# Performance work log

Measured on AMD Instinct MI355X. Metric: run time of the kernel, lower is better.

Reference implementation:

```python
import jax, jax.numpy as jnp
import numpy as np

N = 20000   # nodes
E = 200000  # edges / 1-cells
D = 128     # feature dim
NNZ = 400000
L = 3       # conv layers


def setup_inputs() -> dict:
    key = jax.random.key(0)
    ks = jax.random.split(key, 16)
    s = 1.0 / np.sqrt(D)
    return {
        "x": jax.random.normal(ks[0], (N, D), jnp.float32),
        "xe": jax.random.normal(ks[1], (E, D), jnp.float32),
        "gnn_W": jax.random.normal(ks[2], (L, D, D), jnp.float32) * s,
        "cwnn_W0": jax.random.normal(ks[3], (L, D, D), jnp.float32) * s,
        "cwnn_W1": jax.random.normal(ks[4], (L, D, D), jnp.float32) * s,
        "cwnn_W2": jax.random.normal(ks[5], (L, D, D), jnp.float32) * s,
        "Ldo_val": jax.random.normal(ks[6], (NNZ,), jnp.float32) * 0.1,
        "Lup_val": jax.random.normal(ks[7], (NNZ,), jnp.float32) * 0.1,
        "edges": jax.random.randint(ks[8], (2, E), 0, N, jnp.int32),
        "row": jax.random.randint(ks[9], (E,), 0, N, jnp.int32),
        "col": jax.random.randint(ks[10], (E,), 0, N, jnp.int32),
        "Ldo_idx": jax.random.randint(ks[11], (2, NNZ), 0, E, jnp.int32),
        "Lup_idx": jax.random.randint(ks[12], (2, NNZ), 0, E, jnp.int32),
    }


def _spmm(idx, val, h, n_rows):
    # sparse (COO) matrix @ dense: out[r] = sum_k val[k] * h[idx_col[k]] for idx_row[k]==r
    msgs = val[:, None] * h[idx[1]]             # [nnz, D]
    return jax.ops.segment_sum(msgs, idx[0], num_segments=n_rows)


def reference(x, xe, gnn_W, cwnn_W0, cwnn_W1, cwnn_W2, Ldo_val, Lup_val,
              edges, row, col, Ldo_idx, Lup_idx):
    n = x.shape[0]
    src, dst = edges[0], edges[1]

    # --- GNN over nodes: h' = (h + scatter_sum(h[src] -> dst)) @ W ---
    h = x
    for i in range(gnn_W.shape[0]):
        agg = jax.ops.segment_sum(h[src], dst, num_segments=n)
        h = (h + agg) @ gnn_W[i]
        if i < gnn_W.shape[0] - 1:
            h = jax.nn.relu(h)
    h = jax.nn.relu(h)  # .relu() in CellNetwork.forward

    # --- CWNN over cells: he' = he@W0 + Ldo@(he@W1) + Lup@(he@W2) ---
    he = xe
    for i in range(cwnn_W0.shape[0]):
        he = (he @ cwnn_W0[i]
              + _spmm(Ldo_idx, Ldo_val, he @ cwnn_W1[i], he.shape[0])
              + _spmm(Lup_idx, Lup_val, he @ cwnn_W2[i], he.shape[0]))
        if i < cwnn_W0.shape[0] - 1:
            he = jax.nn.relu(he)
    he = jax.nn.relu(he)  # .relu() in CellNetwork.forward

    # --- dual scatter-add of cell features to nodes + concat ---
    xed = (jax.ops.segment_sum(he, row, num_segments=n)
           + jax.ops.segment_sum(he, col, num_segments=n))
    return jnp.concatenate([h, xed], axis=-1)  # [N, 2D]
```

## Files before the change

kernel.cpp:

```cpp
#include <hip/hip_runtime.h>
#include <cstddef>
#include <cstdint>


using bf16x8 = __attribute__((ext_vector_type(8))) short;
using f32x4  = __attribute__((ext_vector_type(4))) float;
typedef unsigned short u16;
typedef unsigned int   u32;

static inline int cdiv_h(int a, int b){ return (a + b - 1) / b; }

__device__ inline float bflo(u32 u){ return __uint_as_float(u << 16); }
__device__ inline float bfhi(u32 u){ return __uint_as_float(u & 0xFFFF0000u); }
__device__ inline u32 f2bf(float f){
  u32 u = __float_as_uint(f);
  return (u + 0x7FFFu + ((u >> 16) & 1u)) >> 16;
}
__device__ inline u32 pack2(float a, float b){ return f2bf(a) | (f2bf(b) << 16); }


__global__ void hist_key(const int* __restrict__ keys, int* __restrict__ counts, int n){
  int i = blockIdx.x * blockDim.x + threadIdx.x;
  if (i < n) atomicAdd(&counts[keys[i]], 1);
}

__global__ void hist_two(const int* __restrict__ a, const int* __restrict__ b,
                         int* __restrict__ counts, int n){
  int i = blockIdx.x * blockDim.x + threadIdx.x;
  if (i < n){ atomicAdd(&counts[a[i]], 1); atomicAdd(&counts[b[i]], 1); }
}

#define SCAN_CHUNK 2048

__global__ void scan_local(const int* __restrict__ cnt, int* __restrict__ offs,
                           int* __restrict__ partials, int n){
  __shared__ int sd[256];
  int t = threadIdx.x;
  int base = blockIdx.x * SCAN_CHUNK + t * 8;
  int v[8]; int sum = 0;
  #pragma unroll
  for (int i = 0; i < 8; i++){ int idx = base + i; v[i] = (idx < n) ? cnt[idx] : 0; sum += v[i]; }
  sd[t] = sum; __syncthreads();
  for (int off = 1; off < 256; off <<= 1){
    int x = (t >= off) ? sd[t - off] : 0;
    __syncthreads();
    sd[t] += x;
    __syncthreads();
  }
  if (t == 255) partials[blockIdx.x] = sd[255];
  int run = sd[t] - sum;
  #pragma unroll
  for (int i = 0; i < 8; i++){ int idx = base + i; if (idx < n) offs[idx] = run; run += v[i]; }
}

__global__ void scan_partials_k(int* partials, int nb){
  __shared__ int sd[256];
  int t = threadIdx.x;
  int orig = (t < nb) ? partials[t] : 0;
  sd[t] = orig; __syncthreads();
  for (int off = 1; off < 256; off <<= 1){
    int x = (t >= off) ? sd[t - off] : 0;
    __syncthreads();
    sd[t] += x;
    __syncthreads();
  }
  if (t < nb) partials[t] = sd[t] - orig;
}

__global__ void scan_add(int* __restrict__ offs, const int* __restrict__ partials,
                         int n, int total){
  int i = blockIdx.x * blockDim.x + threadIdx.x;
  if (i < n) offs[i] += partials[i / SCAN_CHUNK];
  if (i == 0) offs[n] = total;
}

__global__ void fill_plain(const int* __restrict__ keys, const int* __restrict__ vals,
                           int* __restrict__ cursor, int* __restrict__ ent, int n){
  int i = blockIdx.x * blockDim.x + threadIdx.x;
  if (i < n){ int p = atomicAdd(&cursor[keys[i]], 1); ent[p] = vals[i]; }
}

__global__ void fill_wval(const int* __restrict__ rows, const int* __restrict__ cols,
                          const float* __restrict__ v, int* __restrict__ cursor,
                          int* __restrict__ entc, float* __restrict__ entv, int n){
  int i = blockIdx.x * blockDim.x + threadIdx.x;
  if (i < n){
    int p = atomicAdd(&cursor[rows[i]], 1);
    entc[p] = cols[i]; entv[p] = v[i];
  }
}

__global__ void fill_two(const int* __restrict__ a, const int* __restrict__ b,
                         int* __restrict__ cursor, int* __restrict__ ent, int n){
  int i = blockIdx.x * blockDim.x + threadIdx.x;
  if (i < n){
    int p = atomicAdd(&cursor[a[i]], 1); ent[p] = i;
    int q = atomicAdd(&cursor[b[i]], 1); ent[q] = i;
  }
}


__global__ void gather_f32(const float* __restrict__ src, float* __restrict__ out,
                           const int* __restrict__ offs, const int* __restrict__ ent,
                           const float* __restrict__ selfsrc, int nrows){
  int r = blockIdx.x * 8 + (threadIdx.x >> 5);
  if (r >= nrows) return;
  int d4 = (threadIdx.x & 31) * 4;
  float4 acc0, acc1 = make_float4(0.f, 0.f, 0.f, 0.f);
  acc0 = *(const float4*)&selfsrc[(size_t)r * 128 + d4];
  int b = offs[r], e = offs[r + 1];
  int j = b;
  for (; j + 1 < e; j += 2){
    int c0 = ent[j], c1 = ent[j + 1];
    float4 s0 = *(const float4*)&src[(size_t)c0 * 128 + d4];
    float4 s1 = *(const float4*)&src[(size_t)c1 * 128 + d4];
    acc0.x += s0.x; acc0.y += s0.y; acc0.z += s0.z; acc0.w += s0.w;
    acc1.x += s1.x; acc1.y += s1.y; acc1.z += s1.z; acc1.w += s1.w;
  }
  if (j < e){
    int c = ent[j];
    float4 s = *(const float4*)&src[(size_t)c * 128 + d4];
    acc0.x += s.x; acc0.y += s.y; acc0.z += s.z; acc0.w += s.w;
  }
  acc0.x += acc1.x; acc0.y += acc1.y; acc0.z += acc1.z; acc0.w += acc1.w;
  *(float4*)&out[(size_t)r * 128 + d4] = acc0;
}


__global__ void gather_bf16(const u16* __restrict__ src, u16* __restrict__ out,
                            const int* __restrict__ offs, const int* __restrict__ ent,
                            const float* __restrict__ evals, int nrows){
  int r = blockIdx.x * 8 + (threadIdx.x >> 5);
  if (r >= nrows) return;
  int d4 = (threadIdx.x & 31) * 4;
  float a0=0.f,a1=0.f,a2=0.f,a3=0.f, b0=0.f,b1=0.f,b2=0.f,b3=0.f;
  int b = offs[r], e = offs[r + 1];
  int j = b;
  for (; j + 1 < e; j += 2){
    int c0 = ent[j], c1 = ent[j + 1];
    float w0 = evals[j], w1 = evals[j + 1];
    uint2 s0 = *(const uint2*)&src[(size_t)c0 * 128 + d4];
    uint2 s1 = *(const uint2*)&src[(size_t)c1 * 128 + d4];
    a0 += w0 * bflo(s0.x); a1 += w0 * bfhi(s0.x); a2 += w0 * bflo(s0.y); a3 += w0 * bfhi(s0.y);
    b0 += w1 * bflo(s1.x); b1 += w1 * bfhi(s1.x); b2 += w1 * bflo(s1.y); b3 += w1 * bfhi(s1.y);
  }
  if (j < e){
    int c = ent[j];
    float w = evals[j];
    uint2 s = *(const uint2*)&src[(size_t)c * 128 + d4];
    a0 += w * bflo(s.x); a1 += w * bfhi(s.x); a2 += w * bflo(s.y); a3 += w * bfhi(s.y);
  }
  a0 += b0; a1 += b1; a2 += b2; a3 += b3;
  uint2 o; o.x = pack2(a0, a1); o.y = pack2(a2, a3);
  *(uint2*)&out[(size_t)r * 128 + d4] = o;
}

__global__ void gather_final(const u16* __restrict__ src, float* __restrict__ out,
                             const int* __restrict__ offs, const int* __restrict__ ent,
                             int nrows, int ldout){
  int r = blockIdx.x * 8 + (threadIdx.x >> 5);
  if (r >= nrows) return;
  int d4 = (threadIdx.x & 31) * 4;
  float a0=0.f,a1=0.f,a2=0.f,a3=0.f, b0=0.f,b1=0.f,b2=0.f,b3=0.f;
  int b = offs[r], e = offs[r + 1];
  int j = b;
  for (; j + 1 < e; j += 2){
    int c0 = ent[j], c1 = ent[j + 1];
    uint2 s0 = *(const uint2*)&src[(size_t)c0 * 128 + d4];
    uint2 s1 = *(const uint2*)&src[(size_t)c1 * 128 + d4];
    a0 += bflo(s0.x); a1 += bfhi(s0.x); a2 += bflo(s0.y); a3 += bfhi(s0.y);
    b0 += bflo(s1.x); b1 += bfhi(s1.x); b2 += bflo(s1.y); b3 += bfhi(s1.y);
  }
  if (j < e){
    int c = ent[j];
    uint2 s = *(const uint2*)&src[(size_t)c * 128 + d4];
    a0 += bflo(s.x); a1 += bfhi(s.x); a2 += bflo(s.y); a3 += bfhi(s.y);
  }
  float4 o = make_float4(a0 + b0, a1 + b1, a2 + b2, a3 + b3);
  *(float4*)&out[(size_t)r * ldout + d4] = o;
}


__global__ void cvt_f32_bf16(const float* __restrict__ src, u16* __restrict__ dst, int n8){
  int i = blockIdx.x * blockDim.x + threadIdx.x;
  if (i >= n8) return;
  const float4* s = (const float4*)(src + (size_t)i * 8);
  float4 a = s[0], c = s[1];
  *(uint4*)(dst + (size_t)i * 8) =
      make_uint4(pack2(a.x, a.y), pack2(a.z, a.w), pack2(c.x, c.y), pack2(c.z, c.w));
}


__global__ __launch_bounds__(256) void gemm_f32(
    const float* __restrict__ in, const float* __restrict__ W,
    float* __restrict__ out, int M, int ldout){
  __shared__ float sA[32][132];
  __shared__ float sW[32][128];
  int t  = threadIdx.x;
  int m0 = blockIdx.x * 128;
  int rg = t >> 4;
  int cg = t & 15;
  float acc[8][8];
  #pragma unroll
  for (int i = 0; i < 8; i++)
    #pragma unroll
    for (int j = 0; j < 8; j++) acc[i][j] = 0.f;

  for (int kc = 0; kc < 128; kc += 32){
    #pragma unroll
    for (int ii = 0; ii < 4; ii++){
      int s  = t + ii * 256;
      int r  = s >> 3;
      int k4 = (s & 7) << 2;
      int gr = m0 + r;
      float4 v = (gr < M) ? *(const float4*)&in[(size_t)gr * 128 + kc + k4]
                          : make_float4(0.f, 0.f, 0.f, 0.f);
      sA[k4 + 0][r] = v.x; sA[k4 + 1][r] = v.y; sA[k4 + 2][r] = v.z; sA[k4 + 3][r] = v.w;
    }
    #pragma unroll
    for (int ii = 0; ii < 4; ii++){
      int s  = t + ii * 256;
      int kr = s >> 5;
      int c4 = (s & 31) << 2;
      *(float4*)&sW[kr][c4] = *(const float4*)&W[(size_t)(kc + kr) * 128 + c4];
    }
    __syncthreads();
    #pragma unroll
    for (int k = 0; k < 32; k++){
      float4 a0 = *(const float4*)&sA[k][rg * 8];
      float4 a1 = *(const float4*)&sA[k][rg * 8 + 4];
      float4 w0 = *(const float4*)&sW[k][cg * 8];
      float4 w1 = *(const float4*)&sW[k][cg * 8 + 4];
      float a[8] = {a0.x, a0.y, a0.z, a0.w, a1.x, a1.y, a1.z, a1.w};
      float w[8] = {w0.x, w0.y, w0.z, w0.w, w1.x, w1.y, w1.z, w1.w};
      #pragma unroll
      for (int i = 0; i < 8; i++)
        #pragma unroll
        for (int j = 0; j < 8; j++)
          acc[i][j] = fmaf(a[i], w[j], acc[i][j]);
    }
    __syncthreads();
  }
  #pragma unroll
  for (int i = 0; i < 8; i++){
    int gr = m0 + rg * 8 + i;
    if (gr >= M) continue;
    float* op = out + (size_t)gr * ldout + cg * 8;
    #pragma unroll
    for (int jj = 0; jj < 8; jj += 4){
      float4 o = make_float4(fmaxf(acc[i][jj], 0.f), fmaxf(acc[i][jj + 1], 0.f),
                             fmaxf(acc[i][jj + 2], 0.f), fmaxf(acc[i][jj + 3], 0.f));
      *(float4*)&op[jj] = o;
    }
  }
}


template<int NS>
__global__ __launch_bounds__(256) void gemm_mfma(
    const u16* __restrict__ A0, const u16* __restrict__ A1, const u16* __restrict__ A2,
    const u16* __restrict__ Wa, const u16* __restrict__ Wb, const u16* __restrict__ Wc,
    u16* __restrict__ out, int M){
  __shared__ __align__(16) u16 sA[128 * 40];
  __shared__ __align__(16) u16 sW[128 * 40];
  const int t    = threadIdx.x;
  const int m0   = blockIdx.x * 128;
  const int wid  = t >> 6;
  const int lane = t & 63;
  const int l16  = lane & 15;
  const int kg   = lane >> 4;
  const int nW   = t & 127;
  const int kq   = t >> 7;

  f32x4 acc[2][8];
  #pragma unroll
  for (int i = 0; i < 2; i++)
    #pragma unroll
    for (int j = 0; j < 8; j++) acc[i][j] = (f32x4){0.f, 0.f, 0.f, 0.f};

  #pragma unroll 1
  for (int s = 0; s < NS; s++){
    const u16* A = (s == 0) ? A0 : (s == 1) ? A1 : A2;
    const u16* W = (s == 0) ? Wa : (s == 1) ? Wb : Wc;
    #pragma unroll 1
    for (int kc = 0; kc < 128; kc += 32){
      #pragma unroll
      for (int ii = 0; ii < 2; ii++){
        int sl = t + ii * 256;
        int r  = sl >> 2;
        int q  = sl & 3;
        int gr = m0 + r;
        uint4 v = make_uint4(0u, 0u, 0u, 0u);
        if (gr < M) v = *(const uint4*)&A[(size_t)gr * 128 + kc + q * 8];
        *(uint4*)&sA[r * 40 + q * 8] = v;
      }
      {
        __align__(16) u16 wt[16];
        #pragma unroll
        for (int kk = 0; kk < 16; kk++)
          wt[kk] = W[(size_t)(kc + kq * 16 + kk) * 128 + nW];
        *(uint4*)&sW[nW * 40 + kq * 16]     = *(uint4*)&wt[0];
        *(uint4*)&sW[nW * 40 + kq * 16 + 8] = *(uint4*)&wt[8];
      }
      __syncthreads();
      bf16x8 af0 = *(const bf16x8*)&sA[(wid * 32 +      l16) * 40 + kg * 8];
      bf16x8 af1 = *(const bf16x8*)&sA[(wid * 32 + 16 + l16) * 40 + kg * 8];
      #pragma unroll
      for (int ct = 0; ct < 8; ct++){
        bf16x8 bq = *(const bf16x8*)&sW[(ct * 16 + l16) * 40 + kg * 8];
        acc[0][ct] = __builtin_amdgcn_mfma_f32_16x16x32_bf16(af0, bq, acc[0][ct], 0, 0, 0);
        acc[1][ct] = __builtin_amdgcn_mfma_f32_16x16x32_bf16(af1, bq, acc[1][ct], 0, 0, 0);
      }
      __syncthreads();
    }
  }
  #pragma unroll
  for (int rt = 0; rt < 2; rt++){
    #pragma unroll
    for (int reg = 0; reg < 4; reg++){
      int row = m0 + wid * 32 + rt * 16 + kg * 4 + reg;
      if (row < M){
        #pragma unroll
        for (int ct = 0; ct < 8; ct++){
          float v = fmaxf(acc[rt][ct][reg], 0.f);
          out[(size_t)row * 128 + ct * 16 + l16] = (u16)f2bf(v);
        }
      }
    }
  }
}


extern "C" void kernel_launch(void* const* d_in, const int* in_sizes, int n_in,
                              void* d_out, int out_size, void* d_ws, size_t ws_size,
                              hipStream_t stream){
  const float* x    = (const float*)d_in[0];
  const float* xe   = (const float*)d_in[1];
  const float* gW   = (const float*)d_in[2];
  const float* W0   = (const float*)d_in[3];
  const float* W1   = (const float*)d_in[4];
  const float* W2   = (const float*)d_in[5];
  const float* ldoV = (const float*)d_in[6];
  const float* lupV = (const float*)d_in[7];
  const int*   edges= (const int*)d_in[8];
  const int*   rowi = (const int*)d_in[9];
  const int*   coli = (const int*)d_in[10];
  const int*   ldoI = (const int*)d_in[11];
  const int*   lupI = (const int*)d_in[12];
  (void)n_in; (void)out_size;

  const int D   = 128;
  const int N   = in_sizes[0] / D;
  const int E   = in_sizes[1] / D;
  const int NNZ = in_sizes[6];
  const int L   = in_sizes[2] / (D * D);

  const int* srcN = edges;
  const int* dstN = edges + E;
  const int* ldoR = ldoI;   const int* ldoC = ldoI + NNZ;
  const int* lupR = lupI;   const int* lupC = lupI + NNZ;

  size_t off = 0;
  auto carve = [&](size_t bytes) -> void* {
    void* p = (char*)d_ws + off;
    off += (bytes + 255) & ~(size_t)255;
    return p;
  };
  const size_t EBH = (size_t)E * D * 2;
  u16* EA  = (u16*)carve(EBH);
  u16* EC  = (u16*)carve(EBH);
  u16* EG1 = (u16*)carve(EBH);
  u16* EG2 = (u16*)carve(EBH);
  float* hA = (float*)carve((size_t)N * D * 4);
  float* hB = (float*)carve((size_t)N * D * 4);
  int* offs_g = (int*)carve((size_t)(N + 1) * 4);
  int* cnt_g  = (int*)carve((size_t)N * 4);
  int* ent_g  = (int*)carve((size_t)E * 4);
  int* offs_d = (int*)carve((size_t)(E + 1) * 4);
  int* cnt_d  = (int*)carve((size_t)E * 4);
  int* entc_d = (int*)carve((size_t)NNZ * 4);
  float* entv_d = (float*)carve((size_t)NNZ * 4);
  int* offs_u = (int*)carve((size_t)(E + 1) * 4);
  int* cnt_u  = (int*)carve((size_t)E * 4);
  int* entc_u = (int*)carve((size_t)NNZ * 4);
  float* entv_u = (float*)carve((size_t)NNZ * 4);
  int* offs_f = (int*)carve((size_t)(N + 1) * 4);
  int* cnt_f  = (int*)carve((size_t)N * 4);
  int* ent_f  = (int*)carve((size_t)2 * E * 4);
  int* partials = (int*)carve(256 * 4);
  if (off > ws_size) return;

  const size_t DD = (size_t)D * D;
  u16* WB0 = (u16*)hA;
  u16* WB1 = WB0 + (size_t)L * DD;
  u16* WB2 = WB1 + (size_t)L * DD;

  auto scan3 = [&](int* cnt, int* offs, int n, int total){
    int nb = (n + SCAN_CHUNK - 1) / SCAN_CHUNK;
    scan_local<<<nb, 256, 0, stream>>>(cnt, offs, partials, n);
    scan_partials_k<<<1, 256, 0, stream>>>(partials, nb);
    scan_add<<<cdiv_h(n, 256), 256, 0, stream>>>(offs, partials, n, total);
  };

  hipMemsetAsync(cnt_g, 0, (size_t)N * 4, stream);
  hist_key<<<cdiv_h(E, 256), 256, 0, stream>>>(dstN, cnt_g, E);
  scan3(cnt_g, offs_g, N, E);
  hipMemcpyAsync(cnt_g, offs_g, (size_t)N * 4, hipMemcpyDeviceToDevice, stream);
  fill_plain<<<cdiv_h(E, 256), 256, 0, stream>>>(dstN, srcN, cnt_g, ent_g, E);

  hipMemsetAsync(cnt_d, 0, (size_t)E * 4, stream);
  hist_key<<<cdiv_h(NNZ, 256), 256, 0, stream>>>(ldoR, cnt_d, NNZ);
  scan3(cnt_d, offs_d, E, NNZ);
  hipMemcpyAsync(cnt_d, offs_d, (size_t)E * 4, hipMemcpyDeviceToDevice, stream);
  fill_wval<<<cdiv_h(NNZ, 256), 256, 0, stream>>>(ldoR, ldoC, ldoV, cnt_d, entc_d, entv_d, NNZ);

  hipMemsetAsync(cnt_u, 0, (size_t)E * 4, stream);
  hist_key<<<cdiv_h(NNZ, 256), 256, 0, stream>>>(lupR, cnt_u, NNZ);
  scan3(cnt_u, offs_u, E, NNZ);
  hipMemcpyAsync(cnt_u, offs_u, (size_t)E * 4, hipMemcpyDeviceToDevice, stream);
  fill_wval<<<cdiv_h(NNZ, 256), 256, 0, stream>>>(lupR, lupC, lupV, cnt_u, entc_u, entv_u, NNZ);

  hipMemsetAsync(cnt_f, 0, (size_t)N * 4, stream);
  hist_two<<<cdiv_h(E, 256), 256, 0, stream>>>(rowi, coli, cnt_f, E);
  scan3(cnt_f, offs_f, N, 2 * E);
  hipMemcpyAsync(cnt_f, offs_f, (size_t)N * 4, hipMemcpyDeviceToDevice, stream);
  fill_two<<<cdiv_h(E, 256), 256, 0, stream>>>(rowi, coli, cnt_f, ent_f, E);

  const float* hcur = x;
  for (int i = 0; i < L; i++){
    gather_f32<<<cdiv_h(N, 8), 256, 0, stream>>>(hcur, hA, offs_g, ent_g, hcur, N);
    float* hdst = (i == L - 1) ? (float*)d_out : hB;
    int ldo = (i == L - 1) ? 256 : 128;
    gemm_f32<<<cdiv_h(N, 128), 256, 0, stream>>>(hA, gW + (size_t)i * DD, hdst, N, ldo);
    hcur = hB;
  }

  cvt_f32_bf16<<<cdiv_h(E * D / 8, 256), 256, 0, stream>>>(xe, EA, E * D / 8);
  cvt_f32_bf16<<<cdiv_h((int)(L * DD) / 8, 256), 256, 0, stream>>>(W0, WB0, (int)(L * DD) / 8);
  cvt_f32_bf16<<<cdiv_h((int)(L * DD) / 8, 256), 256, 0, stream>>>(W1, WB1, (int)(L * DD) / 8);
  cvt_f32_bf16<<<cdiv_h((int)(L * DD) / 8, 256), 256, 0, stream>>>(W2, WB2, (int)(L * DD) / 8);

  u16* Acur = EA;
  u16* Aalt = EC;
  for (int i = 0; i < L; i++){
    gather_bf16<<<cdiv_h(E, 8), 256, 0, stream>>>(Acur, EG1, offs_d, entc_d, entv_d, E);
    gather_bf16<<<cdiv_h(E, 8), 256, 0, stream>>>(Acur, EG2, offs_u, entc_u, entv_u, E);
    gemm_mfma<3><<<cdiv_h(E, 128), 256, 0, stream>>>(
        Acur, EG1, EG2, WB0 + i * DD, WB1 + i * DD, WB2 + i * DD, Aalt, E);
    u16* tmp = Acur; Acur = Aalt; Aalt = tmp;
  }

  gather_final<<<cdiv_h(N, 8), 256, 0, stream>>>(Acur, (float*)d_out + 128, offs_f, ent_f,
                                                 N, 256);
}
```

Baseline: 943.5 us.

## Batch CSR preprocessing, fuse dual SpMM gathers, pretranspose weights, retile node GEMM

Merges the four histogram, scan and fill passes into single multi-segment kernels, which cuts launch count and removes the device-to-device cursor copies. Fuses the Ldo and Lup bf16 gathers into one launch that uses 16 threads per row with 16-byte loads. Pre-transposes the CWNN weights to bf16 once so the MFMA GEMM loads W tiles with vector reads instead of strided scalar loads. Halves the fp32 node GEMM row tile to 64 so more blocks run on the GPU. The combined kernels are larger and their atomics contend within one launch.

```diff
diff --git a/kernel.cpp b/kernel.cpp
--- a/kernel.cpp
+++ b/kernel.cpp
@@ -17,29 +17,47 @@
   return (u + 0x7FFFu + ((u >> 16) & 1u)) >> 16;
 }
 __device__ inline u32 pack2(float a, float b){ return f2bf(a) | (f2bf(b) << 16); }
-
-
-__global__ void hist_key(const int* __restrict__ keys, int* __restrict__ counts, int n){
+__device__ inline void acc8(float* a, uint4 s, float w){
+  a[0] += w * bflo(s.x); a[1] += w * bfhi(s.x);
+  a[2] += w * bflo(s.y); a[3] += w * bfhi(s.y);
+  a[4] += w * bflo(s.z); a[5] += w * bfhi(s.z);
+  a[6] += w * bflo(s.w); a[7] += w * bfhi(s.w);
+}
+
+
+__global__ void hist_all(const int* __restrict__ ldoR, const int* __restrict__ lupR,
+                         const int* __restrict__ dstN,
+                         const int* __restrict__ rowi, const int* __restrict__ coli,
+                         int* __restrict__ cnt_d, int* __restrict__ cnt_u,
+                         int* __restrict__ cnt_g, int* __restrict__ cnt_f,
+                         int nnz, int ne){
   int i = blockIdx.x * blockDim.x + threadIdx.x;
-  if (i < n) atomicAdd(&counts[keys[i]], 1);
-}
-
-__global__ void hist_two(const int* __restrict__ a, const int* __restrict__ b,
-                         int* __restrict__ counts, int n){
-  int i = blockIdx.x * blockDim.x + threadIdx.x;
-  if (i < n){ atomicAdd(&counts[a[i]], 1); atomicAdd(&counts[b[i]], 1); }
+  if (i < nnz){
+    atomicAdd(&cnt_d[ldoR[i]], 1);
+    atomicAdd(&cnt_u[lupR[i]], 1);
+  }
+  if (i < ne){
+    atomicAdd(&cnt_g[dstN[i]], 1);
+    atomicAdd(&cnt_f[rowi[i]], 1);
+    atomicAdd(&cnt_f[coli[i]], 1);
+  }
 }
 
 #define SCAN_CHUNK 2048
 
-__global__ void scan_local(const int* __restrict__ cnt, int* __restrict__ offs,
-                           int* __restrict__ partials, int n){
+__global__ void scan_local_multi(const int* __restrict__ cnt, int* __restrict__ offs,
+                                 int* __restrict__ partials, int n, int nb,
+                                 int Sc, int So){
+  int seg = blockIdx.x / nb;
+  int lb  = blockIdx.x % nb;
+  const int* c = cnt + (size_t)seg * Sc;
+  int* o = offs + (size_t)seg * So;
   __shared__ int sd[256];
   int t = threadIdx.x;
-  int base = blockIdx.x * SCAN_CHUNK + t * 8;
+  int base = lb * SCAN_CHUNK + t * 8;
   int v[8]; int sum = 0;
   #pragma unroll
-  for (int i = 0; i < 8; i++){ int idx = base + i; v[i] = (idx < n) ? cnt[idx] : 0; sum += v[i]; }
+  for (int i = 0; i < 8; i++){ int idx = base + i; v[i] = (idx < n) ? c[idx] : 0; sum += v[i]; }
   sd[t] = sum; __syncthreads();
   for (int off = 1; off < 256; off <<= 1){
     int x = (t >= off) ? sd[t - off] : 0;
@@ -47,16 +65,17 @@
     sd[t] += x;
     __syncthreads();
   }
-  if (t == 255) partials[blockIdx.x] = sd[255];
+  if (t == 255) partials[seg * 256 + lb] = sd[255];
   int run = sd[t] - sum;
   #pragma unroll
-  for (int i = 0; i < 8; i++){ int idx = base + i; if (idx < n) offs[idx] = run; run += v[i]; }
-}
-
-__global__ void scan_partials_k(int* partials, int nb){
+  for (int i = 0; i < 8; i++){ int idx = base + i; if (idx < n) o[idx] = run; run += v[i]; }
+}
+
+__global__ void scan_partials_multi(int* partials, int nb){
   __shared__ int sd[256];
+  int seg = blockIdx.x;
   int t = threadIdx.x;
-  int orig = (t < nb) ? partials[t] : 0;
+  int orig = (t < nb) ? partials[seg * 256 + t] : 0;
   sd[t] = orig; __syncthreads();
   for (int off = 1; off < 256; off <<= 1){
     int x = (t >= off) ? sd[t - off] : 0;
@@ -64,38 +83,43 @@
     sd[t] += x;
     __syncthreads();
   }
-  if (t < nb) partials[t] = sd[t] - orig;
-}
-
-__global__ void scan_add(int* __restrict__ offs, const int* __restrict__ partials,
-                         int n, int total){
+  if (t < nb) partials[seg * 256 + t] = sd[t] - orig;
+}
+
+__global__ void scan_add_multi(int* __restrict__ offs, int* __restrict__ cnt,
+                               const int* __restrict__ partials,
+                               int n, int nbAdd, int Sc, int So, int tot0, int tot1){
+  int seg = blockIdx.x / nbAdd;
+  int il  = (blockIdx.x % nbAdd) * blockDim.x + threadIdx.x;
+  int* o = offs + (size_t)seg * So;
+  int* c = cnt + (size_t)seg * Sc;
+  if (il < n){
+    int v = o[il] + partials[seg * 256 + il / SCAN_CHUNK];
+    o[il] = v; c[il] = v;
+  }
+  if (il == 0) o[n] = seg ? tot1 : tot0;
+}
+
+__global__ void fill_all(const int* __restrict__ ldoR, const int* __restrict__ ldoC,
+                         const float* __restrict__ ldoV,
+                         const int* __restrict__ lupR, const int* __restrict__ lupC,
+                         const float* __restrict__ lupV,
+                         const int* __restrict__ srcN, const int* __restrict__ dstN,
+                         const int* __restrict__ rowi, const int* __restrict__ coli,
+                         int* __restrict__ cur_d, int* __restrict__ entc_d, float* __restrict__ entv_d,
+                         int* __restrict__ cur_u, int* __restrict__ entc_u, float* __restrict__ entv_u,
+                         int* __restrict__ cur_g, int* __restrict__ ent_g,
+                         int* __restrict__ cur_f, int* __restrict__ ent_f,
+                         int nnz, int ne){
   int i = blockIdx.x * blockDim.x + threadIdx.x;
-  if (i < n) offs[i] += partials[i / SCAN_CHUNK];
-  if (i == 0) offs[n] = total;
-}
-
-__global__ void fill_plain(const int* __restrict__ keys, const int* __restrict__ vals,
-                           int* __restrict__ cursor, int* __restrict__ ent, int n){
-  int i = blockIdx.x * blockDim.x + threadIdx.x;
-  if (i < n){ int p = atomicAdd(&cursor[keys[i]], 1); ent[p] = vals[i]; }
-}
-
-__global__ void fill_wval(const int* __restrict__ rows, const int* __restrict__ cols,
-                          const float* __restrict__ v, int* __restrict__ cursor,
-                          int* __restrict__ entc, float* __restrict__ entv, int n){
-  int i = blockIdx.x * blockDim.x + threadIdx.x;
-  if (i < n){
-    int p = atomicAdd(&cursor[rows[i]], 1);
-    entc[p] = cols[i]; entv[p] = v[i];
-  }
-}
-
-__global__ void fill_two(const int* __restrict__ a, const int* __restrict__ b,
-                         int* __restrict__ cursor, int* __restrict__ ent, int n){
-  int i = blockIdx.x * blockDim.x + threadIdx.x;
-  if (i < n){
-    int p = atomicAdd(&cursor[a[i]], 1); ent[p] = i;
-    int q = atomicAdd(&cursor[b[i]], 1); ent[q] = i;
+  if (i < nnz){
+    int p = atomicAdd(&cur_d[ldoR[i]], 1); entc_d[p] = ldoC[i]; entv_d[p] = ldoV[i];
+    int q = atomicAdd(&cur_u[lupR[i]], 1); entc_u[q] = lupC[i]; entv_u[q] = lupV[i];
+  }
+  if (i < ne){
+    int p = atomicAdd(&cur_g[dstN[i]], 1); ent_g[p] = srcN[i];
+    int a = atomicAdd(&cur_f[rowi[i]], 1); ent_f[a] = i;
+    int b = atomicAdd(&cur_f[coli[i]], 1); ent_f[b] = i;
   }
 }
 
@@ -127,57 +151,72 @@
 }
 
 
-__global__ void gather_bf16(const u16* __restrict__ src, u16* __restrict__ out,
-                            const int* __restrict__ offs, const int* __restrict__ ent,
-                            const float* __restrict__ evals, int nrows){
-  int r = blockIdx.x * 8 + (threadIdx.x >> 5);
-  if (r >= nrows) return;
-  int d4 = (threadIdx.x & 31) * 4;
-  float a0=0.f,a1=0.f,a2=0.f,a3=0.f, b0=0.f,b1=0.f,b2=0.f,b3=0.f;
-  int b = offs[r], e = offs[r + 1];
-  int j = b;
-  for (; j + 1 < e; j += 2){
-    int c0 = ent[j], c1 = ent[j + 1];
-    float w0 = evals[j], w1 = evals[j + 1];
-    uint2 s0 = *(const uint2*)&src[(size_t)c0 * 128 + d4];
-    uint2 s1 = *(const uint2*)&src[(size_t)c1 * 128 + d4];
-    a0 += w0 * bflo(s0.x); a1 += w0 * bfhi(s0.x); a2 += w0 * bflo(s0.y); a3 += w0 * bfhi(s0.y);
-    b0 += w1 * bflo(s1.x); b1 += w1 * bfhi(s1.x); b2 += w1 * bflo(s1.y); b3 += w1 * bfhi(s1.y);
-  }
-  if (j < e){
-    int c = ent[j];
-    float w = evals[j];
-    uint2 s = *(const uint2*)&src[(size_t)c * 128 + d4];
-    a0 += w * bflo(s.x); a1 += w * bfhi(s.x); a2 += w * bflo(s.y); a3 += w * bfhi(s.y);
-  }
-  a0 += b0; a1 += b1; a2 += b2; a3 += b3;
-  uint2 o; o.x = pack2(a0, a1); o.y = pack2(a2, a3);
-  *(uint2*)&out[(size_t)r * 128 + d4] = o;
-}
+__global__ void gather_bf16_dual(const u16* __restrict__ src,
+                                 u16* __restrict__ out1, u16* __restrict__ out2,
+                                 const int* __restrict__ offs_d, const int* __restrict__ entc_d,
+                                 const float* __restrict__ entv_d,
+                                 const int* __restrict__ offs_u, const int* __restrict__ entc_u,
+                                 const float* __restrict__ entv_u, int nrows){
+  int gr = blockIdx.x * 16 + (threadIdx.x >> 4);
+  if (gr >= 2 * nrows) return;
+  bool up = gr >= nrows;
+  int r = up ? gr - nrows : gr;
+  const int*   offs = up ? offs_u : offs_d;
+  const int*   entc = up ? entc_u : entc_d;
+  const float* entv = up ? entv_u : entv_d;
+  u16* out = up ? out2 : out1;
+  int d8 = (threadIdx.x & 15) * 8;
+  float a[8] = {0,0,0,0,0,0,0,0};
+  float b[8] = {0,0,0,0,0,0,0,0};
+  int be = offs[r], en = offs[r + 1];
+  int j = be;
+  for (; j + 1 < en; j += 2){
+    int c0 = entc[j], c1 = entc[j + 1];
+    float w0 = entv[j], w1 = entv[j + 1];
+    uint4 s0 = *(const uint4*)&src[(size_t)c0 * 128 + d8];
+    uint4 s1 = *(const uint4*)&src[(size_t)c1 * 128 + d8];
+    acc8(a, s0, w0);
+    acc8(b, s1, w1);
+  }
+  if (j < en){
+    int c = entc[j];
+    uint4 s = *(const uint4*)&src[(size_t)c * 128 + d8];
+    acc8(a, s, entv[j]);
+  }
+  uint4 o;
+  o.x = pack2(a[0] + b[0], a[1] + b[1]);
+  o.y = pack2(a[2] + b[2], a[3] + b[3]);
+  o.z = pack2(a[4] + b[4], a[5] + b[5]);
+  o.w = pack2(a[6] + b[6], a[7] + b[7]);
+  *(uint4*)&out[(size_t)r * 128 + d8] = o;
+}
+
 
 __global__ void gather_final(const u16* __restrict__ src, float* __restrict__ out,
                              const int* __restrict__ offs, const int* __restrict__ ent,
                              int nrows, int ldout){
-  int r = blockIdx.x * 8 + (threadIdx.x >> 5);
+  int r = blockIdx.x * 16 + (threadIdx.x >> 4);
   if (r >= nrows) return;
-  int d4 = (threadIdx.x & 31) * 4;
-  float a0=0.f,a1=0.f,a2=0.f,a3=0.f, b0=0.f,b1=0.f,b2=0.f,b3=0.f;
-  int b = offs[r], e = offs[r + 1];
-  int j = b;
-  for (; j + 1 < e; j += 2){
+  int d8 = (threadIdx.x & 15) * 8;
+  float a[8] = {0,0,0,0,0,0,0,0};
+  float b[8] = {0,0,0,0,0,0,0,0};
+  int be = offs[r], en = offs[r + 1];
+  int j = be;
+  for (; j + 1 < en; j += 2){
     int c0 = ent[j], c1 = ent[j + 1];
-    uint2 s0 = *(const uint2*)&src[(size_t)c0 * 128 + d4];
-    uint2 s1 = *(const uint2*)&src[(size_t)c1 * 128 + d4];
-    a0 += bflo(s0.x); a1 += bfhi(s0.x); a2 += bflo(s0.y); a3 += bfhi(s0.y);
-    b0 += bflo(s1.x); b1 += bfhi(s1.x); b2 += bflo(s1.y); b3 += bfhi(s1.y);
-  }
-  if (j < e){
+    uint4 s0 = *(const uint4*)&src[(size_t)c0 * 128 + d8];
+    uint4 s1 = *(const uint4*)&src[(size_t)c1 * 128 + d8];
+    acc8(a, s0, 1.0f);
+    acc8(b, s1, 1.0f);
+  }
+  if (j < en){
     int c = ent[j];
-    uint2 s = *(const uint2*)&src[(size_t)c * 128 + d4];
-    a0 += bflo(s.x); a1 += bfhi(s.x); a2 += bflo(s.y); a3 += bfhi(s.y);
-  }
-  float4 o = make_float4(a0 + b0, a1 + b1, a2 + b2, a3 + b3);
-  *(float4*)&out[(size_t)r * ldout + d4] = o;
+    uint4 s = *(const uint4*)&src[(size_t)c * 128 + d8];
+    acc8(a, s, 1.0f);
+  }
+  float* op = out + (size_t)r * ldout + d8;
+  *(float4*)&op[0] = make_float4(a[0]+b[0], a[1]+b[1], a[2]+b[2], a[3]+b[3]);
+  *(float4*)&op[4] = make_float4(a[4]+b[4], a[5]+b[5], a[6]+b[6], a[7]+b[7]);
 }
 
 
@@ -191,24 +230,45 @@
 }
 
 
+__global__ void transp_w(const float* __restrict__ W0, const float* __restrict__ W1,
+                         const float* __restrict__ W2, u16* __restrict__ WT, int L){
+  int tid = blockIdx.x * blockDim.x + threadIdx.x;
+  int total = 3 * L * 8 * 128;
+  if (tid >= total) return;
+  int n = tid & 127;
+  int g = (tid >> 7) & 7;
+  int m = tid >> 10;
+  const float* src = (m < L) ? (W0 + (size_t)m * 16384)
+                   : (m < 2 * L) ? (W1 + (size_t)(m - L) * 16384)
+                   : (W2 + (size_t)(m - 2 * L) * 16384);
+  u16* dst = WT + (size_t)m * 16384;
+  u16 tmp[16];
+  #pragma unroll
+  for (int kk = 0; kk < 16; kk++)
+    tmp[kk] = (u16)f2bf(src[(size_t)(g * 16 + kk) * 128 + n]);
+  *(uint4*)&dst[(size_t)n * 128 + g * 16]     = *(uint4*)&tmp[0];
+  *(uint4*)&dst[(size_t)n * 128 + g * 16 + 8] = *(uint4*)&tmp[8];
+}
+
+
 __global__ __launch_bounds__(256) void gemm_f32(
     const float* __restrict__ in, const float* __restrict__ W,
     float* __restrict__ out, int M, int ldout){
-  __shared__ float sA[32][132];
+  __shared__ float sA[32][68];
   __shared__ float sW[32][128];
   int t  = threadIdx.x;
-  int m0 = blockIdx.x * 128;
+  int m0 = blockIdx.x * 64;
   int rg = t >> 4;
   int cg = t & 15;
-  float acc[8][8];
-  #pragma unroll
-  for (int i = 0; i < 8; i++)
+  float acc[4][8];
+  #pragma unroll
+  for (int i = 0; i < 4; i++)
     #pragma unroll
     for (int j = 0; j < 8; j++) acc[i][j] = 0.f;
 
   for (int kc = 0; kc < 128; kc += 32){
     #pragma unroll
-    for (int ii = 0; ii < 4; ii++){
+    for (int ii = 0; ii < 2; ii++){
       int s  = t + ii * 256;
       int r  = s >> 3;
       int k4 = (s & 7) << 2;
@@ -227,14 +287,13 @@
     __syncthreads();
     #pragma unroll
     for (int k = 0; k < 32; k++){
-      float4 a0 = *(const float4*)&sA[k][rg * 8];
-      float4 a1 = *(const float4*)&sA[k][rg * 8 + 4];
+      float4 a0 = *(const float4*)&sA[k][rg * 4];
       float4 w0 = *(const float4*)&sW[k][cg * 8];
       float4 w1 = *(const float4*)&sW[k][cg * 8 + 4];
-      float a[8] = {a0.x, a0.y, a0.z, a0.w, a1.x, a1.y, a1.z, a1.w};
+      float a[4] = {a0.x, a0.y, a0.z, a0.w};
       float w[8] = {w0.x, w0.y, w0.z, w0.w, w1.x, w1.y, w1.z, w1.w};
       #pragma unroll
-      for (int i = 0; i < 8; i++)
+      for (int i = 0; i < 4; i++)
         #pragma unroll
         for (int j = 0; j < 8; j++)
           acc[i][j] = fmaf(a[i], w[j], acc[i][j]);
@@ -242,8 +301,8 @@
     __syncthreads();
   }
   #pragma unroll
-  for (int i = 0; i < 8; i++){
-    int gr = m0 + rg * 8 + i;
+  for (int i = 0; i < 4; i++){
+    int gr = m0 + rg * 4 + i;
     if (gr >= M) continue;
     float* op = out + (size_t)gr * ldout + cg * 8;
     #pragma unroll
@@ -280,8 +339,8 @@
 
   #pragma unroll 1
   for (int s = 0; s < NS; s++){
-    const u16* A = (s == 0) ? A0 : (s == 1) ? A1 : A2;
-    const u16* W = (s == 0) ? Wa : (s == 1) ? Wb : Wc;
+    const u16* A  = (s == 0) ? A0 : (s == 1) ? A1 : A2;
+    const u16* WT = (s == 0) ? Wa : (s == 1) ? Wb : Wc;
     #pragma unroll 1
     for (int kc = 0; kc < 128; kc += 32){
       #pragma unroll
@@ -294,14 +353,8 @@
         if (gr < M) v = *(const uint4*)&A[(size_t)gr * 128 + kc + q * 8];
         *(uint4*)&sA[r * 40 + q * 8] = v;
       }
-      {
-        __align__(16) u16 wt[16];
-        #pragma unroll
-        for (int kk = 0; kk < 16; kk++)
-          wt[kk] = W[(size_t)(kc + kq * 16 + kk) * 128 + nW];
-        *(uint4*)&sW[nW * 40 + kq * 16]     = *(uint4*)&wt[0];
-        *(uint4*)&sW[nW * 40 + kq * 16 + 8] = *(uint4*)&wt[8];
-      }
+      *(uint4*)&sW[nW * 40 + kq * 16]     = *(const uint4*)&WT[(size_t)nW * 128 + kc + kq * 16];
+      *(uint4*)&sW[nW * 40 + kq * 16 + 8] = *(const uint4*)&WT[(size_t)nW * 128 + kc + kq * 16 + 8];
       __syncthreads();
       bf16x8 af0 = *(const bf16x8*)&sA[(wid * 32 +      l16) * 40 + kg * 8];
       bf16x8 af1 = *(const bf16x8*)&sA[(wid * 32 + 16 + l16) * 40 + kg * 8];
@@ -373,83 +426,80 @@
   u16* EG2 = (u16*)carve(EBH);
   float* hA = (float*)carve((size_t)N * D * 4);
   float* hB = (float*)carve((size_t)N * D * 4);
-  int* offs_g = (int*)carve((size_t)(N + 1) * 4);
-  int* cnt_g  = (int*)carve((size_t)N * 4);
+  int* cnts   = (int*)carve((size_t)(2 * E + 2 * N) * 4);
+  int* cnt_d  = cnts;
+  int* cnt_u  = cnts + E;
+  int* cnt_g  = cnts + 2 * E;
+  int* cnt_f  = cnts + 2 * E + N;
+  const int SoE = E + 64;
+  const int SoN = N + 64;
+  int* offsE  = (int*)carve((size_t)2 * SoE * 4);
+  int* offs_d = offsE;
+  int* offs_u = offsE + SoE;
+  int* offsN  = (int*)carve((size_t)2 * SoN * 4);
+  int* offs_g = offsN;
+  int* offs_f = offsN + SoN;
   int* ent_g  = (int*)carve((size_t)E * 4);
-  int* offs_d = (int*)carve((size_t)(E + 1) * 4);
-  int* cnt_d  = (int*)carve((size_t)E * 4);
   int* entc_d = (int*)carve((size_t)NNZ * 4);
   float* entv_d = (float*)carve((size_t)NNZ * 4);
-  int* offs_u = (int*)carve((size_t)(E + 1) * 4);
-  int* cnt_u  = (int*)carve((size_t)E * 4);
   int* entc_u = (int*)carve((size_t)NNZ * 4);
   float* entv_u = (float*)carve((size_t)NNZ * 4);
-  int* offs_f = (int*)carve((size_t)(N + 1) * 4);
-  int* cnt_f  = (int*)carve((size_t)N * 4);
   int* ent_f  = (int*)carve((size_t)2 * E * 4);
-  int* partials = (int*)carve(256 * 4);
+  int* partials = (int*)carve(512 * 4);
   if (off > ws_size) return;
 
   const size_t DD = (size_t)D * D;
-  u16* WB0 = (u16*)hA;
-  u16* WB1 = WB0 + (size_t)L * DD;
-  u16* WB2 = WB1 + (size_t)L * DD;
-
-  auto scan3 = [&](int* cnt, int* offs, int n, int total){
-    int nb = (n + SCAN_CHUNK - 1) / SCAN_CHUNK;
-    scan_local<<<nb, 256, 0, stream>>>(cnt, offs, partials, n);
-    scan_partials_k<<<1, 256, 0, stream>>>(partials, nb);
-    scan_add<<<cdiv_h(n, 256), 256, 0, stream>>>(offs, partials, n, total);
-  };
-
-  hipMemsetAsync(cnt_g, 0, (size_t)N * 4, stream);
-  hist_key<<<cdiv_h(E, 256), 256, 0, stream>>>(dstN, cnt_g, E);
-  scan3(cnt_g, offs_g, N, E);
-  hipMemcpyAsync(cnt_g, offs_g, (size_t)N * 4, hipMemcpyDeviceToDevice, stream);
-  fill_plain<<<cdiv_h(E, 256), 256, 0, stream>>>(dstN, srcN, cnt_g, ent_g, E);
-
-  hipMemsetAsync(cnt_d, 0, (size_t)E * 4, stream);
-  hist_key<<<cdiv_h(NNZ, 256), 256, 0, stream>>>(ldoR, cnt_d, NNZ);
-  scan3(cnt_d, offs_d, E, NNZ);
-  hipMemcpyAsync(cnt_d, offs_d, (size_t)E * 4, hipMemcpyDeviceToDevice, stream);
-  fill_wval<<<cdiv_h(NNZ, 256), 256, 0, stream>>>(ldoR, ldoC, ldoV, cnt_d, entc_d, entv_d, NNZ);
-
-  hipMemsetAsync(cnt_u, 0, (size_t)E * 4, stream);
-  hist_key<<<cdiv_h(NNZ, 256), 256, 0, stream>>>(lupR, cnt_u, NNZ);
-  scan3(cnt_u, offs_u, E, NNZ);
-  hipMemcpyAsync(cnt_u, offs_u, (size_t)E * 4, hipMemcpyDeviceToDevice, stream);
-  fill_wval<<<cdiv_h(NNZ, 256), 256, 0, stream>>>(lupR, lupC, lupV, cnt_u, entc_u, entv_u, NNZ);
-
-  hipMemsetAsync(cnt_f, 0, (size_t)N * 4, stream);
-  hist_two<<<cdiv_h(E, 256), 256, 0, stream>>>(rowi, coli, cnt_f, E);
-  scan3(cnt_f, offs_f, N, 2 * E);
-  hipMemcpyAsync(cnt_f, offs_f, (size_t)N * 4, hipMemcpyDeviceToDevice, stream);
-  fill_two<<<cdiv_h(E, 256), 256, 0, stream>>>(rowi, coli, cnt_f, ent_f, E);
+  u16* WTb = (u16*)hA;
+  u16* WB0 = WTb;
+  u16* WB1 = WTb + (size_t)L * DD;
+  u16* WB2 = WTb + (size_t)2 * L * DD;
+
+  hipMemsetAsync(cnts, 0, (size_t)(2 * E + 2 * N) * 4, stream);
+  hist_all<<<cdiv_h(NNZ, 256), 256, 0, stream>>>(ldoR, lupR, dstN, rowi, coli,
+                                                 cnt_d, cnt_u, cnt_g, cnt_f, NNZ, E);
+  {
+    int nbE = cdiv_h(E, SCAN_CHUNK);
+    scan_local_multi<<<2 * nbE, 256, 0, stream>>>(cnt_d, offs_d, partials, E, nbE, E, SoE);
+    scan_partials_multi<<<2, 256, 0, stream>>>(partials, nbE);
+    int nbAdd = cdiv_h(E, 256);
+    scan_add_multi<<<2 * nbAdd, 256, 0, stream>>>(offs_d, cnt_d, partials, E, nbAdd,
+                                                  E, SoE, NNZ, NNZ);
+  }
+  {
+    int nbN = cdiv_h(N, SCAN_CHUNK);
+    scan_local_multi<<<2 * nbN, 256, 0, stream>>>(cnt_g, offs_g, partials, N, nbN, N, SoN);
+    scan_partials_multi<<<2, 256, 0, stream>>>(partials, nbN);
+    int nbAdd = cdiv_h(N, 256);
+    scan_add_multi<<<2 * nbAdd, 256, 0, stream>>>(offs_g, cnt_g, partials, N, nbAdd,
+                                                  N, SoN, E, 2 * E);
+  }
+  fill_all<<<cdiv_h(NNZ, 256), 256, 0, stream>>>(
+      ldoR, ldoC, ldoV, lupR, lupC, lupV, srcN, dstN, rowi, coli,
+      cnt_d, entc_d, entv_d, cnt_u, entc_u, entv_u,
+      cnt_g, ent_g, cnt_f, ent_f, NNZ, E);
 
   const float* hcur = x;
   for (int i = 0; i < L; i++){
     gather_f32<<<cdiv_h(N, 8), 256, 0, stream>>>(hcur, hA, offs_g, ent_g, hcur, N);
     float* hdst = (i == L - 1) ? (float*)d_out : hB;
     int ldo = (i == L - 1) ? 256 : 128;
-    gemm_f32<<<cdiv_h(N, 128), 256, 0, stream>>>(hA, gW + (size_t)i * DD, hdst, N, ldo);
+    gemm_f32<<<cdiv_h(N, 64), 256, 0, stream>>>(hA, gW + (size_t)i * DD, hdst, N, ldo);
     hcur = hB;
   }
 
   cvt_f32_bf16<<<cdiv_h(E * D / 8, 256), 256, 0, stream>>>(xe, EA, E * D / 8);
-  cvt_f32_bf16<<<cdiv_h((int)(L * DD) / 8, 256), 256, 0, stream>>>(W0, WB0, (int)(L * DD) / 8);
-  cvt_f32_bf16<<<cdiv_h((int)(L * DD) / 8, 256), 256, 0, stream>>>(W1, WB1, (int)(L * DD) / 8);
-  cvt_f32_bf16<<<cdiv_h((int)(L * DD) / 8, 256), 256, 0, stream>>>(W2, WB2, (int)(L * DD) / 8);
+  transp_w<<<cdiv_h(3 * L * 8 * 128, 256), 256, 0, stream>>>(W0, W1, W2, WTb, L);
 
   u16* Acur = EA;
   u16* Aalt = EC;
   for (int i = 0; i < L; i++){
-    gather_bf16<<<cdiv_h(E, 8), 256, 0, stream>>>(Acur, EG1, offs_d, entc_d, entv_d, E);
-    gather_bf16<<<cdiv_h(E, 8), 256, 0, stream>>>(Acur, EG2, offs_u, entc_u, entv_u, E);
+    gather_bf16_dual<<<cdiv_h(2 * E, 16), 256, 0, stream>>>(
+        Acur, EG1, EG2, offs_d, entc_d, entv_d, offs_u, entc_u, entv_u, E);
     gemm_mfma<3><<<cdiv_h(E, 128), 256, 0, stream>>>(
         Acur, EG1, EG2, WB0 + i * DD, WB1 + i * DD, WB2 + i * DD, Aalt, E);
     u16* tmp = Acur; Acur = Aalt; Aalt = tmp;
   }
 
-  gather_final<<<cdiv_h(N, 8), 256, 0, stream>>>(Acur, (float*)d_out + 128, offs_f, ent_f,
-                                                 N, 256);
-}
+  gather_final<<<cdiv_h(N, 16), 256, 0, stream>>>(Acur, (float*)d_out + 128, offs_f, ent_f,
+                                                  N, 256);
+}
```

New measurement: 798.2 us. 15.4% less time.
